# Performance work log

Hardware: AMD Instinct MI355X
Metric: run time of the kernel (lower is better)

Reference implementation:

```python
import jax, jax.numpy as jnp
import numpy as np

NUM_ITEM = 50000
D = 64
LN_EPS = 1e-5


def _l2norm(x, axis=-1):
    # F.normalize: x / max(||x||, eps)
    n = jnp.sqrt(jnp.sum(x * x, axis=axis, keepdims=True))
    return x / jnp.maximum(n, 1e-12)


def _mlp(x, w1, b1, w2, b2, w3, b3):
    h = jax.nn.relu(x @ w1.T + b1)
    h = jax.nn.relu(h @ w2.T + b2)
    return h @ w3.T + b3


def setup_inputs() -> dict:
    key = jax.random.key(0)
    ks = jax.random.split(key, 20)
    d_c, d_t = 1024, 768
    inp = {
        'seq_modify': jax.random.randint(ks[0], (1024, 50), 0, NUM_ITEM + 1),
        'content_feature': jax.random.normal(ks[1], (NUM_ITEM, d_c), jnp.float32),
        'text_feature': jax.random.normal(ks[2], (NUM_ITEM, d_t), jnp.float32),
        'cf_feature': jax.random.normal(ks[3], (NUM_ITEM, D), jnp.float32),
        'item_embeddings': jax.random.normal(ks[4], (NUM_ITEM, D), jnp.float32) * 0.05,
        'c_w1': jax.random.normal(ks[5], (d_c, d_c), jnp.float32) * (1.0 / np.sqrt(d_c)),
        'c_b1': jnp.zeros((d_c,), jnp.float32),
        'c_w2': jax.random.normal(ks[6], (256, d_c), jnp.float32) * (1.0 / np.sqrt(d_c)),
        'c_b2': jnp.zeros((256,), jnp.float32),
        'c_w3': jax.random.normal(ks[7], (D, 256), jnp.float32) * (1.0 / np.sqrt(256)),
        'c_b3': jnp.zeros((D,), jnp.float32),
        't_w1': jax.random.normal(ks[8], (d_t, d_t), jnp.float32) * (1.0 / np.sqrt(d_t)),
        't_b1': jnp.zeros((d_t,), jnp.float32),
        't_w2': jax.random.normal(ks[9], (256, d_t), jnp.float32) * (1.0 / np.sqrt(d_t)),
        't_b2': jnp.zeros((256,), jnp.float32),
        't_w3': jax.random.normal(ks[10], (D, 256), jnp.float32) * (1.0 / np.sqrt(256)),
        't_b3': jnp.zeros((D,), jnp.float32),
        'cf_w': jax.random.normal(ks[11], (D, D), jnp.float32) * (1.0 / np.sqrt(D)),
        'cf_b': jnp.zeros((D,), jnp.float32),
        'wq': jax.random.normal(ks[12], (D, D), jnp.float32) * (1.0 / np.sqrt(D)),
        'wk': jax.random.normal(ks[13], (D, D), jnp.float32) * (1.0 / np.sqrt(D)),
        'wv': jax.random.normal(ks[14], (D, D), jnp.float32) * (1.0 / np.sqrt(D)),
    }
    return inp


def reference(seq_modify, content_feature, text_feature, cf_feature, item_embeddings,
              c_w1, c_b1, c_w2, c_b2, c_w3, c_b3,
              t_w1, t_b1, t_w2, t_b2, t_w3, t_b3,
              cf_w, cf_b, wq, wk, wv):
    # padding index num_item -> 0 (masked_fill in torch forward)
    seq = jnp.where(seq_modify == NUM_ITEM, 0, seq_modify)  # [bs, n_token]

    # modality encoders over the full catalog (content/text L2-normalized in __init__)
    c_emb = _mlp(_l2norm(content_feature), c_w1, c_b1, c_w2, c_b2, c_w3, c_b3)  # [N, 64]
    t_emb = _mlp(_l2norm(text_feature), t_w1, t_b1, t_w2, t_b2, t_w3, t_b3)    # [N, 64]
    cf_emb = cf_feature @ cf_w.T + cf_b                                         # [N, 64]
    id_emb = item_embeddings                                                    # [N, 64]

    # gather per-token modality embeddings and stack modals: [bs, n, 4, 64]
    feats = jnp.stack([c_emb[seq], t_emb[seq], cf_emb[seq], id_emb[seq]], axis=-2)
    bs, n_tok, n_modal, d = feats.shape

    x = _l2norm(feats).reshape(-1, n_modal, d)  # [bs*n, 4, 64]

    # selfAttention: LayerNorm (no affine) -> q,k,v -> softmax attn -> mean pool
    mu = jnp.mean(x, axis=-1, keepdims=True)
    var = jnp.mean((x - mu) ** 2, axis=-1, keepdims=True)
    xn = (x - mu) / jnp.sqrt(var + LN_EPS)
    q = xn @ wq.T
    k = xn @ wk.T
    v = xn @ wv.T
    attn = jax.nn.softmax(jnp.einsum('bmd,bnd->bmn', q * (d ** -0.5), k), axis=-1)
    fused = jnp.einsum('bmn,bnd->bmd', attn, v).mean(axis=-2)  # [bs*n, 64]
    return fused.reshape(bs, n_tok, d)
```

## Files before the change

### kernel.cpp

```cpp
#include <hip/hip_runtime.h>
#include <hip/hip_bf16.h>
#include <type_traits>

typedef __hip_bfloat16 bf16;
typedef __attribute__((ext_vector_type(8))) short short8;
typedef __attribute__((ext_vector_type(4))) float floatx4;

static constexpr int kNumItem = 50000;

__device__ __forceinline__ float bf2f(const bf16 x) { return __bfloat162float(x); }

union alignas(16) Pack8 {
  bf16 b[8];
  short8 s;
};
union alignas(8) Pack4 {
  bf16 b[4];
  short4 s;
};

__device__ __forceinline__ void async_cp16(const void* g, void* l) {
  __builtin_amdgcn_global_load_lds((const __attribute__((address_space(1))) void*)g,
                                   (__attribute__((address_space(3))) void*)l, 16, 0, 0);
}

__device__ __forceinline__ int xcd_swz(int orig, int nwg) {
  const int nx = 8;
  const int q = nwg / nx, r = nwg % nx;
  const int xcd = orig % nx, loc = orig / nx;
  return (xcd < r ? xcd * (q + 1) : r * (q + 1) + (xcd - r) * q) + loc;
}

__global__ __launch_bounds__(256) void row_invnorm(const float* __restrict__ X,
                                                   float* __restrict__ out,
                                                   int M, int K) {
  const int lane = threadIdx.x & 63;
  const int wave = threadIdx.x >> 6;
  const int row = blockIdx.x * 4 + wave;
  if (row >= M) return;
  const float* xr = X + (size_t)row * K;
  float s = 0.f;
  for (int c = lane * 8; c < K; c += 64 * 8) {
    float4 a = *(const float4*)(xr + c);
    float4 b = *(const float4*)(xr + c + 4);
    s += a.x * a.x + a.y * a.y + a.z * a.z + a.w * a.w;
    s += b.x * b.x + b.y * b.y + b.z * b.z + b.w * b.w;
  }
#pragma unroll
  for (int off = 32; off > 0; off >>= 1) s += __shfl_xor(s, off, 64);
  if (lane == 0) out[row] = 1.0f / fmaxf(sqrtf(s), 1e-12f);
}

__global__ __launch_bounds__(256) void cvt_rows_norm(const float* __restrict__ X,
                                                     bf16* __restrict__ Xb,
                                                     float* __restrict__ out,
                                                     int M, int K) {
  const int lane = threadIdx.x & 63;
  const int wave = threadIdx.x >> 6;
  const int row = blockIdx.x * 4 + wave;
  if (row >= M) return;
  const float* xr = X + (size_t)row * K;
  bf16* dr = Xb + (size_t)row * K;
  float s = 0.f;
  for (int c = lane * 8; c < K; c += 64 * 8) {
    float4 a = *(const float4*)(xr + c);
    float4 b = *(const float4*)(xr + c + 4);
    s += a.x * a.x + a.y * a.y + a.z * a.z + a.w * a.w;
    s += b.x * b.x + b.y * b.y + b.z * b.z + b.w * b.w;
    Pack8 p;
    p.b[0] = __float2bfloat16(a.x); p.b[1] = __float2bfloat16(a.y);
    p.b[2] = __float2bfloat16(a.z); p.b[3] = __float2bfloat16(a.w);
    p.b[4] = __float2bfloat16(b.x); p.b[5] = __float2bfloat16(b.y);
    p.b[6] = __float2bfloat16(b.z); p.b[7] = __float2bfloat16(b.w);
    *(short8*)(void*)(dr + c) = p.s;
  }
#pragma unroll
  for (int off = 32; off > 0; off >>= 1) s += __shfl_xor(s, off, 64);
  if (lane == 0) out[row] = 1.0f / fmaxf(sqrtf(s), 1e-12f);
}

static constexpr int kNWSeg = 10;
struct WPack {
  const float* src[kNWSeg];
  int start4[kNWSeg];
  int total4;
};
__global__ __launch_bounds__(256) void cvt_many(WPack p, bf16* __restrict__ dst) {
  int c = blockIdx.x * 256 + threadIdx.x;
  const int stride = gridDim.x * 256;
  for (; c < p.total4; c += stride) {
    int s = 0;
#pragma unroll
    for (int k = 1; k < kNWSeg; k++)
      if (c >= p.start4[k]) s = k;
    const float4 v = ((const float4*)p.src[s])[c - p.start4[s]];
    Pack4 q;
    q.b[0] = __float2bfloat16(v.x); q.b[1] = __float2bfloat16(v.y);
    q.b[2] = __float2bfloat16(v.z); q.b[3] = __float2bfloat16(v.w);
    *(short4*)(void*)(dst + (size_t)c * 4) = q.s;
  }
}

template <int BM, int BN, typename AT, typename BT, typename CT>
__global__ __launch_bounds__(256) void gemm_bt(const AT* __restrict__ A,
                                               const BT* __restrict__ B,
                                               CT* __restrict__ C,
                                               int M, int N, int K,
                                               const float* __restrict__ rowScale,
                                               const float* __restrict__ bias,
                                               int doRelu) {
  constexpr int BK = 32;
  __shared__ __align__(16) bf16 sA[BM * BK];
  __shared__ __align__(16) bf16 sB[BN * BK];
  const int t = threadIdx.x;
  const int lane = t & 63;
  const int wave = t >> 6;
  constexpr int WN = BN / 64;
  const int wm = wave / WN;
  const int wn = wave % WN;
  const int gx = gridDim.x;
  const int wgid = xcd_swz(blockIdx.y * gx + blockIdx.x, gx * gridDim.y);
  const int m0 = (wgid / gx) * BM;
  const int n0 = (wgid % gx) * BN;
  const int lane16 = lane & 15;
  const int quad = lane >> 4;

  floatx4 acc[4][4];
#pragma unroll
  for (int i = 0; i < 4; i++)
#pragma unroll
    for (int j = 0; j < 4; j++) acc[i][j] = (floatx4)0.0f;

  for (int k0 = 0; k0 < K; k0 += BK) {
#pragma unroll
    for (int it = 0; it < BM / 64; ++it) {
      int c = t + 256 * it;
      int row = c >> 2;
      int col = (c & 3) * 8;
      int gr = m0 + row;
      if (gr > M - 1) gr = M - 1;
      if constexpr (std::is_same_v<AT, bf16>) {
        async_cp16(A + (size_t)gr * K + k0 + col, &sA[c * 8]);
      } else {
        const float* src = A + (size_t)gr * K + k0 + col;
        float4 fa = *(const float4*)src;
        float4 fb = *(const float4*)(src + 4);
        Pack8 p;
        p.b[0] = __float2bfloat16(fa.x); p.b[1] = __float2bfloat16(fa.y);
        p.b[2] = __float2bfloat16(fa.z); p.b[3] = __float2bfloat16(fa.w);
        p.b[4] = __float2bfloat16(fb.x); p.b[5] = __float2bfloat16(fb.y);
        p.b[6] = __float2bfloat16(fb.z); p.b[7] = __float2bfloat16(fb.w);
        *(short8*)(void*)&sA[c * 8] = p.s;
      }
    }
#pragma unroll
    for (int it = 0; it < BN / 64; ++it) {
      int c = t + 256 * it;
      int row = c >> 2;
      int col = (c & 3) * 8;
      int gr = n0 + row;
      if (gr > N - 1) gr = N - 1;
      if constexpr (std::is_same_v<BT, bf16>) {
        async_cp16(B + (size_t)gr * K + k0 + col, &sB[c * 8]);
      } else {
        const float* src = B + (size_t)gr * K + k0 + col;
        float4 fa = *(const float4*)src;
        float4 fb = *(const float4*)(src + 4);
        Pack8 p;
        p.b[0] = __float2bfloat16(fa.x); p.b[1] = __float2bfloat16(fa.y);
        p.b[2] = __float2bfloat16(fa.z); p.b[3] = __float2bfloat16(fa.w);
        p.b[4] = __float2bfloat16(fb.x); p.b[5] = __float2bfloat16(fb.y);
        p.b[6] = __float2bfloat16(fb.z); p.b[7] = __float2bfloat16(fb.w);
        *(short8*)(void*)&sB[c * 8] = p.s;
      }
    }
    __syncthreads();

    short8 afr[4], bfr[4];
#pragma unroll
    for (int i = 0; i < 4; i++)
      afr[i] = *(const short8*)(const void*)&sA[(wm * 64 + i * 16 + lane16) * BK + quad * 8];
#pragma unroll
    for (int j = 0; j < 4; j++)
      bfr[j] = *(const short8*)(const void*)&sB[(wn * 64 + j * 16 + lane16) * BK + quad * 8];
#pragma unroll
    for (int i = 0; i < 4; i++)
#pragma unroll
      for (int j = 0; j < 4; j++)
        acc[i][j] = __builtin_amdgcn_mfma_f32_16x16x32_bf16(afr[i], bfr[j], acc[i][j], 0, 0, 0);
    __syncthreads();
  }

#pragma unroll
  for (int i = 0; i < 4; i++) {
#pragma unroll
    for (int j = 0; j < 4; j++) {
      const int col = n0 + wn * 64 + j * 16 + lane16;
      const float bv = bias ? bias[col] : 0.f;
#pragma unroll
      for (int r = 0; r < 4; r++) {
        const int row = m0 + wm * 64 + i * 16 + quad * 4 + r;
        if (row < M) {
          float v = acc[i][j][r];
          if (rowScale) v *= rowScale[row];
          v += bv;
          if (doRelu) v = v > 0.f ? v : 0.f;
          if constexpr (std::is_same_v<CT, bf16>)
            C[(size_t)row * N + col] = __float2bfloat16(v);
          else
            C[(size_t)row * N + col] = v;
        }
      }
    }
  }
}

template <typename CT>
__global__ __launch_bounds__(512) void gemm_bt2(const bf16* __restrict__ A,
                                                const bf16* __restrict__ B,
                                                CT* __restrict__ C,
                                                int M, int N, int K,
                                                const float* __restrict__ rowScale,
                                                const float* __restrict__ bias,
                                                int doRelu) {
  constexpr int BM = 128, BN = 256, BK = 32;
  __shared__ __align__(16) bf16 sA[BM * BK];
  __shared__ __align__(16) bf16 sB[BN * BK];
  const int t = threadIdx.x;
  const int lane = t & 63;
  const int wave = t >> 6;
  const int wm = wave >> 2;
  const int wn = wave & 3;
  const int gx = gridDim.x;
  const int wgid = xcd_swz(blockIdx.y * gx + blockIdx.x, gx * gridDim.y);
  const int m0 = (wgid / gx) * BM;
  const int n0 = (wgid % gx) * BN;
  const int lane16 = lane & 15;
  const int quad = lane >> 4;

  floatx4 acc[4][4];
#pragma unroll
  for (int i = 0; i < 4; i++)
#pragma unroll
    for (int j = 0; j < 4; j++) acc[i][j] = (floatx4)0.0f;

  for (int k0 = 0; k0 < K; k0 += BK) {
    {
      const int c = t;
      const int row = c >> 2;
      const int col = (c & 3) * 8;
      int gr = m0 + row;
      if (gr > M - 1) gr = M - 1;
      async_cp16(A + (size_t)gr * K + k0 + col, &sA[c * 8]);
    }
#pragma unroll
    for (int it = 0; it < 2; ++it) {
      const int c = t + 512 * it;
      const int row = c >> 2;
      const int col = (c & 3) * 8;
      int gr = n0 + row;
      if (gr > N - 1) gr = N - 1;
      async_cp16(B + (size_t)gr * K + k0 + col, &sB[c * 8]);
    }
    __syncthreads();

    short8 afr[4], bfr[4];
#pragma unroll
    for (int i = 0; i < 4; i++)
      afr[i] = *(const short8*)(const void*)&sA[(wm * 64 + i * 16 + lane16) * BK + quad * 8];
#pragma unroll
    for (int j = 0; j < 4; j++)
      bfr[j] = *(const short8*)(const void*)&sB[(wn * 64 + j * 16 + lane16) * BK + quad * 8];
#pragma unroll
    for (int i = 0; i < 4; i++)
#pragma unroll
      for (int j = 0; j < 4; j++)
        acc[i][j] = __builtin_amdgcn_mfma_f32_16x16x32_bf16(afr[i], bfr[j], acc[i][j], 0, 0, 0);
    __syncthreads();
  }

#pragma unroll
  for (int i = 0; i < 4; i++) {
#pragma unroll
    for (int j = 0; j < 4; j++) {
      const int col = n0 + wn * 64 + j * 16 + lane16;
      const float bv = bias ? bias[col] : 0.f;
#pragma unroll
      for (int r = 0; r < 4; r++) {
        const int row = m0 + wm * 64 + i * 16 + quad * 4 + r;
        if (row < M) {
          float v = acc[i][j][r];
          if (rowScale) v *= rowScale[row];
          v += bv;
          if (doRelu) v = v > 0.f ? v : 0.f;
          if constexpr (std::is_same_v<CT, bf16>)
            C[(size_t)row * N + col] = __float2bfloat16(v);
          else
            C[(size_t)row * N + col] = v;
        }
      }
    }
  }
}

__global__ __launch_bounds__(256) void norm_ln(const bf16* __restrict__ c_emb,
                                               const bf16* __restrict__ t_emb,
                                               const bf16* __restrict__ cf_emb,
                                               const float* __restrict__ id_emb,
                                               bf16* __restrict__ Xn, int nItem) {
  const int gid = blockIdx.x * 256 + threadIdx.x;
  const int row = gid >> 4;
  const int d4 = gid & 15;
  if (row >= nItem * 4) return;
  const int item = row >> 2;
  const int m = row & 3;

  float x[4];
  if (m == 3) {
    const float4 f = *(const float4*)(id_emb + (size_t)item * 64 + d4 * 4);
    x[0] = f.x; x[1] = f.y; x[2] = f.z; x[3] = f.w;
  } else {
    const bf16* src = (m == 0) ? c_emb : (m == 1 ? t_emb : cf_emb);
    Pack4 p;
    p.s = *(const short4*)(const void*)(src + (size_t)item * 64 + d4 * 4);
    x[0] = bf2f(p.b[0]); x[1] = bf2f(p.b[1]); x[2] = bf2f(p.b[2]); x[3] = bf2f(p.b[3]);
  }

  float sm = x[0] + x[1] + x[2] + x[3];
  float ss = x[0] * x[0] + x[1] * x[1] + x[2] * x[2] + x[3] * x[3];
#pragma unroll
  for (int off = 1; off < 16; off <<= 1) {
    sm += __shfl_xor(sm, off, 64);
    ss += __shfl_xor(ss, off, 64);
  }
  const float inv = 1.0f / fmaxf(sqrtf(ss), 1e-12f);
  const float mu = sm * inv * (1.0f / 64.0f);
  const float ex2 = ss * inv * inv * (1.0f / 64.0f);
  const float var = ex2 - mu * mu;
  const float rs = rsqrtf(var + 1e-5f);

  Pack4 o;
#pragma unroll
  for (int c = 0; c < 4; c++) o.b[c] = __float2bfloat16((x[c] * inv - mu) * rs);
  *(short4*)(void*)(Xn + (size_t)row * 64 + d4 * 4) = o.s;
}

__global__ __launch_bounds__(256) void attn4(const float* __restrict__ Q,
                                             const float* __restrict__ K,
                                             const float* __restrict__ V,
                                             float* __restrict__ out, int nGroup) {
  const int t = threadIdx.x;
  const int wave = t >> 6;
  const int lane = t & 63;
  const int sub = lane >> 4;
  const int d4 = lane & 15;
  const int group = blockIdx.x * 4 + wave;
  if (group >= nGroup) return;
  const int item = group * 4 + sub;
  const size_t rb = (size_t)item * 4;

  float4 q4[4], k4[4], v4[4];
#pragma unroll
  for (int m = 0; m < 4; m++) {
    q4[m] = *(const float4*)(Q + (rb + m) * 64 + d4 * 4);
    k4[m] = *(const float4*)(K + (rb + m) * 64 + d4 * 4);
    v4[m] = *(const float4*)(V + (rb + m) * 64 + d4 * 4);
  }

  float p[16];
#pragma unroll
  for (int m = 0; m < 4; m++)
#pragma unroll
    for (int n = 0; n < 4; n++)
      p[m * 4 + n] = q4[m].x * k4[n].x + q4[m].y * k4[n].y +
                     q4[m].z * k4[n].z + q4[m].w * k4[n].w;
#pragma unroll
  for (int off = 1; off < 16; off <<= 1)
#pragma unroll
    for (int i = 0; i < 16; i++) p[i] += __shfl_xor(p[i], off, 64);

  float abar[4] = {0, 0, 0, 0};
#pragma unroll
  for (int m = 0; m < 4; m++) {
    const float s0 = p[m * 4 + 0] * 0.125f, s1 = p[m * 4 + 1] * 0.125f;
    const float s2 = p[m * 4 + 2] * 0.125f, s3 = p[m * 4 + 3] * 0.125f;
    const float mx = fmaxf(fmaxf(s0, s1), fmaxf(s2, s3));
    const float e0 = expf(s0 - mx), e1 = expf(s1 - mx);
    const float e2 = expf(s2 - mx), e3 = expf(s3 - mx);
    const float inv = 1.0f / (e0 + e1 + e2 + e3);
    abar[0] += e0 * inv;
    abar[1] += e1 * inv;
    abar[2] += e2 * inv;
    abar[3] += e3 * inv;
  }

  float4 o;
  o.x = 0.25f * (abar[0] * v4[0].x + abar[1] * v4[1].x + abar[2] * v4[2].x + abar[3] * v4[3].x);
  o.y = 0.25f * (abar[0] * v4[0].y + abar[1] * v4[1].y + abar[2] * v4[2].y + abar[3] * v4[3].y);
  o.z = 0.25f * (abar[0] * v4[0].z + abar[1] * v4[1].z + abar[2] * v4[2].z + abar[3] * v4[3].z);
  o.w = 0.25f * (abar[0] * v4[0].w + abar[1] * v4[1].w + abar[2] * v4[2].w + abar[3] * v4[3].w);
  *(float4*)(out + (size_t)item * 64 + d4 * 4) = o;
}

__global__ __launch_bounds__(256, 4) void fuse_attn2(const int* __restrict__ seq,
                                                     const bf16* __restrict__ c_emb,
                                                     const bf16* __restrict__ t_emb,
                                                     const bf16* __restrict__ cf_emb,
                                                     const float* __restrict__ id_emb,
                                                     const float* __restrict__ wq,
                                                     const float* __restrict__ wk,
                                                     const float* __restrict__ wv,
                                                     float* __restrict__ out, int n_tok) {
  __shared__ __align__(16) float4 swc[3072];
  __shared__ float sxn[4][4][64];
  const int t = threadIdx.x;
  const int lane = t & 63;
  const int wave = t >> 6;

  for (int c = t; c < 3072; c += 256) {
    const int mat = c >> 10, rem = c & 1023, d4 = rem >> 6, j = rem & 63;
    const float* W = (mat == 0) ? wq : (mat == 1 ? wk : wv);
    swc[c] = *(const float4*)(W + j * 64 + d4 * 4);
  }
  __syncthreads();

  const int gw = blockIdx.x * 4 + wave;
  const int gstride = gridDim.x * 4;
  for (int token = gw; token < n_tok; token += gstride) {
    int idx = seq ? seq[token] : token;
    if (idx >= kNumItem || idx < 0) idx = 0;

    float x[4];
    x[0] = bf2f(c_emb[(size_t)idx * 64 + lane]);
    x[1] = bf2f(t_emb[(size_t)idx * 64 + lane]);
    x[2] = bf2f(cf_emb[(size_t)idx * 64 + lane]);
    x[3] = id_emb[(size_t)idx * 64 + lane];

#pragma unroll
    for (int m = 0; m < 4; m++) {
      float sm = x[m], ss = x[m] * x[m];
#pragma unroll
      for (int off = 32; off > 0; off >>= 1) {
        sm += __shfl_xor(sm, off, 64);
        ss += __shfl_xor(ss, off, 64);
      }
      const float inv = 1.0f / fmaxf(sqrtf(ss), 1e-12f);
      const float xh = x[m] * inv;
      const float mu = sm * inv * (1.0f / 64.0f);
      const float ex2 = ss * inv * inv * (1.0f / 64.0f);
      const float var = ex2 - mu * mu;
      const float xn = (xh - mu) * rsqrtf(var + 1e-5f);
      x[m] = xn;
      sxn[wave][m][lane] = xn;
    }

    float q[4] = {0, 0, 0, 0}, kk[4] = {0, 0, 0, 0}, v[4] = {0, 0, 0, 0};
#pragma unroll
    for (int d4 = 0; d4 < 16; d4++) {
      const float4 a = swc[d4 * 64 + lane];
      const float4 b = swc[1024 + d4 * 64 + lane];
      const float4 g = swc[2048 + d4 * 64 + lane];
#pragma unroll
      for (int m = 0; m < 4; m++) {
        const float4 xn4 = *(const float4*)&sxn[wave][m][d4 * 4];
        q[m] += xn4.x * a.x + xn4.y * a.y + xn4.z * a.z + xn4.w * a.w;
        kk[m] += xn4.x * b.x + xn4.y * b.y + xn4.z * b.z + xn4.w * b.w;
        v[m] += xn4.x * g.x + xn4.y * g.y + xn4.z * g.z + xn4.w * g.w;
      }
    }

    float p[16];
#pragma unroll
    for (int m = 0; m < 4; m++)
#pragma unroll
      for (int n = 0; n < 4; n++) p[m * 4 + n] = q[m] * kk[n];
#pragma unroll
    for (int off = 1; off < 64; off <<= 1)
#pragma unroll
      for (int i = 0; i < 16; i++) p[i] += __shfl_xor(p[i], off, 64);

    float abar[4] = {0, 0, 0, 0};
#pragma unroll
    for (int m = 0; m < 4; m++) {
      float s0 = p[m * 4 + 0] * 0.125f, s1 = p[m * 4 + 1] * 0.125f;
      float s2 = p[m * 4 + 2] * 0.125f, s3 = p[m * 4 + 3] * 0.125f;
      float mx = fmaxf(fmaxf(s0, s1), fmaxf(s2, s3));
      float e0 = expf(s0 - mx), e1 = expf(s1 - mx), e2 = expf(s2 - mx), e3 = expf(s3 - mx);
      float inv = 1.0f / (e0 + e1 + e2 + e3);
      abar[0] += e0 * inv;
      abar[1] += e1 * inv;
      abar[2] += e2 * inv;
      abar[3] += e3 * inv;
    }
    const float o =
        0.25f * (abar[0] * v[0] + abar[1] * v[1] + abar[2] * v[2] + abar[3] * v[3]);
    out[(size_t)token * 64 + lane] = o;
  }
}

__global__ __launch_bounds__(256) void gather_out(const int* __restrict__ seq,
                                                  const float* __restrict__ fused,
                                                  float* __restrict__ out, int n_tok) {
  const int gid = blockIdx.x * 256 + threadIdx.x;
  if (gid >= n_tok * 16) return;
  const int token = gid >> 4;
  const int c4 = gid & 15;
  int idx = seq[token];
  if (idx >= kNumItem || idx < 0) idx = 0;
  ((float4*)out)[(size_t)token * 16 + c4] = ((const float4*)fused)[(size_t)idx * 16 + c4];
}

extern "C" void kernel_launch(void* const* d_in, const int* in_sizes, int n_in,
                              void* d_out, int out_size, void* d_ws, size_t ws_size,
                              hipStream_t stream) {
  const int* seq = (const int*)d_in[0];
  const float* content = (const float*)d_in[1];
  const float* text = (const float*)d_in[2];
  const float* cf_feat = (const float*)d_in[3];
  const float* item_emb = (const float*)d_in[4];
  const float* c_w1 = (const float*)d_in[5];
  const float* c_b1 = (const float*)d_in[6];
  const float* c_w2 = (const float*)d_in[7];
  const float* c_b2 = (const float*)d_in[8];
  const float* c_w3 = (const float*)d_in[9];
  const float* c_b3 = (const float*)d_in[10];
  const float* t_w1 = (const float*)d_in[11];
  const float* t_b1 = (const float*)d_in[12];
  const float* t_w2 = (const float*)d_in[13];
  const float* t_b2 = (const float*)d_in[14];
  const float* t_w3 = (const float*)d_in[15];
  const float* t_b3 = (const float*)d_in[16];
  const float* cf_w = (const float*)d_in[17];
  const float* cf_b = (const float*)d_in[18];
  const float* wq = (const float*)d_in[19];
  const float* wk = (const float*)d_in[20];
  const float* wv = (const float*)d_in[21];
  float* out = (float*)d_out;

  const int M = kNumItem;
  const int n_tok = in_sizes[0];

  char* w = (char*)d_ws;
  size_t off = 0;
  auto alloc = [&](size_t bytes) -> void* {
    void* p = w + off;
    off += (bytes + 255) & ~(size_t)255;
    return p;
  };
  float* invn_c = (float*)alloc((size_t)M * 4);
  float* invn_t = (float*)alloc((size_t)M * 4);
  bf16* c_emb = (bf16*)alloc((size_t)M * 64 * 2);
  bf16* t_emb = (bf16*)alloc((size_t)M * 64 * 2);
  bf16* cf_emb = (bf16*)alloc((size_t)M * 64 * 2);
  bf16* H1 = (bf16*)alloc((size_t)M * 1024 * 2);
  bf16* H2 = (bf16*)alloc((size_t)M * 256 * 2);

  const int nw[kNWSeg] = {1024 * 1024, 256 * 1024, 64 * 256, 768 * 768, 256 * 768,
                          64 * 256,    64 * 64,    64 * 64,  64 * 64,   64 * 64};
  int wofs[kNWSeg + 1];
  wofs[0] = 0;
  for (int i = 0; i < kNWSeg; i++) wofs[i + 1] = wofs[i] + nw[i];
  bf16* Wb = (bf16*)alloc((size_t)wofs[kNWSeg] * 2);
  const bool useWb = (off <= ws_size);
  bf16* Ab = (bf16*)alloc((size_t)M * 1024 * 2);
  const bool useAb = useWb && (off <= ws_size);
  float* fusedTab = (float*)alloc((size_t)M * 64 * 4);
  const bool useFused = (off <= ws_size);

  const int R = M * 4;
  bf16* Xn = (bf16*)Ab;
  float* Vbuf = (float*)((char*)Ab + (size_t)R * 64 * 2);
  float* Qbuf = (float*)H1;
  float* Kbuf = (float*)((char*)H1 + (size_t)R * 64 * 4);

  if (useWb) {
    WPack p;
    const float* srcs[kNWSeg] = {c_w1, c_w2, c_w3, t_w1, t_w2, t_w3, cf_w, wq, wk, wv};
    for (int i = 0; i < kNWSeg; i++) {
      p.src[i] = srcs[i];
      p.start4[i] = wofs[i] / 4;
    }
    p.total4 = wofs[kNWSeg] / 4;
    cvt_many<<<dim3(2048), dim3(256), 0, stream>>>(p, Wb);
  }

  if (useAb) {
    cvt_rows_norm<<<dim3((M + 3) / 4), dim3(256), 0, stream>>>(content, Ab, invn_c, M, 1024);
    gemm_bt2<bf16><<<dim3(1024 / 256, (M + 127) / 128), dim3(512), 0, stream>>>(
        Ab, Wb + wofs[0], H1, M, 1024, 1024, invn_c, c_b1, 1);
    gemm_bt2<bf16><<<dim3(1, (M + 127) / 128), dim3(512), 0, stream>>>(
        H1, Wb + wofs[1], H2, M, 256, 1024, nullptr, c_b2, 1);
    gemm_bt<256, 64, bf16, bf16, bf16>
        <<<dim3(1, (M + 255) / 256), dim3(256), 0, stream>>>(
            H2, Wb + wofs[2], c_emb, M, 64, 256, nullptr, c_b3, 0);

    cvt_rows_norm<<<dim3((M + 3) / 4), dim3(256), 0, stream>>>(text, Ab, invn_t, M, 768);
    gemm_bt2<bf16><<<dim3(768 / 256, (M + 127) / 128), dim3(512), 0, stream>>>(
        Ab, Wb + wofs[3], H1, M, 768, 768, invn_t, t_b1, 1);
    gemm_bt2<bf16><<<dim3(1, (M + 127) / 128), dim3(512), 0, stream>>>(
        H1, Wb + wofs[4], H2, M, 256, 768, nullptr, t_b2, 1);
    gemm_bt<256, 64, bf16, bf16, bf16>
        <<<dim3(1, (M + 255) / 256), dim3(256), 0, stream>>>(
            H2, Wb + wofs[5], t_emb, M, 64, 256, nullptr, t_b3, 0);

    gemm_bt<256, 64, float, bf16, bf16>
        <<<dim3(1, (M + 255) / 256), dim3(256), 0, stream>>>(
            cf_feat, Wb + wofs[6], cf_emb, M, 64, 64, nullptr, cf_b, 0);

    norm_ln<<<dim3((R * 16 + 255) / 256), dim3(256), 0, stream>>>(
        c_emb, t_emb, cf_emb, item_emb, Xn, M);
    gemm_bt<256, 64, bf16, bf16, float>
        <<<dim3(1, (R + 255) / 256), dim3(256), 0, stream>>>(
            Xn, Wb + wofs[7], Qbuf, R, 64, 64, nullptr, nullptr, 0);
    gemm_bt<256, 64, bf16, bf16, float>
        <<<dim3(1, (R + 255) / 256), dim3(256), 0, stream>>>(
            Xn, Wb + wofs[8], Kbuf, R, 64, 64, nullptr, nullptr, 0);
    gemm_bt<256, 64, bf16, bf16, float>
        <<<dim3(1, (R + 255) / 256), dim3(256), 0, stream>>>(
            Xn, Wb + wofs[9], Vbuf, R, 64, 64, nullptr, nullptr, 0);
    const int nGroup = (M + 3) / 4;
    attn4<<<dim3((nGroup + 3) / 4), dim3(256), 0, stream>>>(
        Qbuf, Kbuf, Vbuf, fusedTab, nGroup);
    gather_out<<<dim3((n_tok * 16 + 255) / 256), dim3(256), 0, stream>>>(
        seq, fusedTab, out, n_tok);
  } else if (useWb) {
    row_invnorm<<<dim3((M + 3) / 4), dim3(256), 0, stream>>>(content, invn_c, M, 1024);
    row_invnorm<<<dim3((M + 3) / 4), dim3(256), 0, stream>>>(text, invn_t, M, 768);
    gemm_bt<128, 128, float, bf16, bf16>
        <<<dim3(1024 / 128, (M + 127) / 128), dim3(256), 0, stream>>>(
            content, Wb + wofs[0], H1, M, 1024, 1024, invn_c, c_b1, 1);
    gemm_bt<128, 128, bf16, bf16, bf16>
        <<<dim3(256 / 128, (M + 127) / 128), dim3(256), 0, stream>>>(
            H1, Wb + wofs[1], H2, M, 256, 1024, nullptr, c_b2, 1);
    gemm_bt<256, 64, bf16, bf16, bf16>
        <<<dim3(1, (M + 255) / 256), dim3(256), 0, stream>>>(
            H2, Wb + wofs[2], c_emb, M, 64, 256, nullptr, c_b3, 0);
    gemm_bt<128, 128, float, bf16, bf16>
        <<<dim3(768 / 128, (M + 127) / 128), dim3(256), 0, stream>>>(
            text, Wb + wofs[3], H1, M, 768, 768, invn_t, t_b1, 1);
    gemm_bt<128, 128, bf16, bf16, bf16>
        <<<dim3(256 / 128, (M + 127) / 128), dim3(256), 0, stream>>>(
            H1, Wb + wofs[4], H2, M, 256, 768, nullptr, t_b2, 1);
    gemm_bt<256, 64, bf16, bf16, bf16>
        <<<dim3(1, (M + 255) / 256), dim3(256), 0, stream>>>(
            H2, Wb + wofs[5], t_emb, M, 64, 256, nullptr, t_b3, 0);
    gemm_bt<256, 64, float, bf16, bf16>
        <<<dim3(1, (M + 255) / 256), dim3(256), 0, stream>>>(
            cf_feat, Wb + wofs[6], cf_emb, M, 64, 64, nullptr, cf_b, 0);
    if (useFused) {
      fuse_attn2<<<dim3(768), dim3(256), 0, stream>>>(
          nullptr, c_emb, t_emb, cf_emb, item_emb, wq, wk, wv, fusedTab, M);
      gather_out<<<dim3((n_tok * 16 + 255) / 256), dim3(256), 0, stream>>>(
          seq, fusedTab, out, n_tok);
    } else {
      fuse_attn2<<<dim3(768), dim3(256), 0, stream>>>(
          seq, c_emb, t_emb, cf_emb, item_emb, wq, wk, wv, out, n_tok);
    }
  } else {
    row_invnorm<<<dim3((M + 3) / 4), dim3(256), 0, stream>>>(content, invn_c, M, 1024);
    row_invnorm<<<dim3((M + 3) / 4), dim3(256), 0, stream>>>(text, invn_t, M, 768);
    gemm_bt<128, 128, float, float, bf16>
        <<<dim3(1024 / 128, (M + 127) / 128), dim3(256), 0, stream>>>(
            content, c_w1, H1, M, 1024, 1024, invn_c, c_b1, 1);
    gemm_bt<128, 128, bf16, float, bf16>
        <<<dim3(256 / 128, (M + 127) / 128), dim3(256), 0, stream>>>(
            H1, c_w2, H2, M, 256, 1024, nullptr, c_b2, 1);
    gemm_bt<256, 64, bf16, float, bf16>
        <<<dim3(1, (M + 255) / 256), dim3(256), 0, stream>>>(
            H2, c_w3, c_emb, M, 64, 256, nullptr, c_b3, 0);
    gemm_bt<128, 128, float, float, bf16>
        <<<dim3(768 / 128, (M + 127) / 128), dim3(256), 0, stream>>>(
            text, t_w1, H1, M, 768, 768, invn_t, t_b1, 1);
    gemm_bt<128, 128, bf16, float, bf16>
        <<<dim3(256 / 128, (M + 127) / 128), dim3(256), 0, stream>>>(
            H1, t_w2, H2, M, 256, 768, nullptr, t_b2, 1);
    gemm_bt<256, 64, bf16, float, bf16>
        <<<dim3(1, (M + 255) / 256), dim3(256), 0, stream>>>(
            H2, t_w3, t_emb, M, 64, 256, nullptr, t_b3, 0);
    gemm_bt<256, 64, float, float, bf16>
        <<<dim3(1, (M + 255) / 256), dim3(256), 0, stream>>>(
            cf_feat, cf_w, cf_emb, M, 64, 64, nullptr, cf_b, 0);
    fuse_attn2<<<dim3(768), dim3(256), 0, stream>>>(
        seq, c_emb, t_emb, cf_emb, item_emb, wq, wk, wv, out, n_tok);
  }
}
```

Measured before the change: 1.034 ms.

## Double-buffer GEMM LDS tiles and merge Q/K projections into one bf16 GEMM

Both GEMM kernels now use two LDS buffers per operand, so the next K-tile is prefetched while MFMAs run on the current one, and one barrier per iteration is dropped. Separately, the Q and K projections become a single GEMM with N=128 over the contiguous wq/wk weights, writing bf16 instead of fp32, and attn4 reads the interleaved QK buffer. This cuts one launch and halves the Q/K intermediate traffic. The cost is doubled LDS usage, which may lower occupancy, and Q/K now carry bf16 precision.

```diff
diff --git a/kernel.cpp b/kernel.cpp
--- a/kernel.cpp
+++ b/kernel.cpp
@@ -110,8 +110,8 @@
                                                const float* __restrict__ bias,
                                                int doRelu) {
   constexpr int BK = 32;
-  __shared__ __align__(16) bf16 sA[BM * BK];
-  __shared__ __align__(16) bf16 sB[BN * BK];
+  __shared__ __align__(16) bf16 sA[2][BM * BK];
+  __shared__ __align__(16) bf16 sB[2][BN * BK];
   const int t = threadIdx.x;
   const int lane = t & 63;
   const int wave = t >> 6;
@@ -125,13 +125,7 @@
   const int lane16 = lane & 15;
   const int quad = lane >> 4;
 
-  floatx4 acc[4][4];
-#pragma unroll
-  for (int i = 0; i < 4; i++)
-#pragma unroll
-    for (int j = 0; j < 4; j++) acc[i][j] = (floatx4)0.0f;
-
-  for (int k0 = 0; k0 < K; k0 += BK) {
+  auto stageA = [&](int k0, bf16* dst) {
 #pragma unroll
     for (int it = 0; it < BM / 64; ++it) {
       int c = t + 256 * it;
@@ -140,7 +134,7 @@
       int gr = m0 + row;
       if (gr > M - 1) gr = M - 1;
       if constexpr (std::is_same_v<AT, bf16>) {
-        async_cp16(A + (size_t)gr * K + k0 + col, &sA[c * 8]);
+        async_cp16(A + (size_t)gr * K + k0 + col, dst + c * 8);
       } else {
         const float* src = A + (size_t)gr * K + k0 + col;
         float4 fa = *(const float4*)src;
@@ -150,9 +144,11 @@
         p.b[2] = __float2bfloat16(fa.z); p.b[3] = __float2bfloat16(fa.w);
         p.b[4] = __float2bfloat16(fb.x); p.b[5] = __float2bfloat16(fb.y);
         p.b[6] = __float2bfloat16(fb.z); p.b[7] = __float2bfloat16(fb.w);
-        *(short8*)(void*)&sA[c * 8] = p.s;
+        *(short8*)(void*)(dst + c * 8) = p.s;
       }
     }
+  };
+  auto stageB = [&](int k0, bf16* dst) {
 #pragma unroll
     for (int it = 0; it < BN / 64; ++it) {
       int c = t + 256 * it;
@@ -161,7 +157,7 @@
       int gr = n0 + row;
       if (gr > N - 1) gr = N - 1;
       if constexpr (std::is_same_v<BT, bf16>) {
-        async_cp16(B + (size_t)gr * K + k0 + col, &sB[c * 8]);
+        async_cp16(B + (size_t)gr * K + k0 + col, dst + c * 8);
       } else {
         const float* src = B + (size_t)gr * K + k0 + col;
         float4 fa = *(const float4*)src;
@@ -171,24 +167,41 @@
         p.b[2] = __float2bfloat16(fa.z); p.b[3] = __float2bfloat16(fa.w);
         p.b[4] = __float2bfloat16(fb.x); p.b[5] = __float2bfloat16(fb.y);
         p.b[6] = __float2bfloat16(fb.z); p.b[7] = __float2bfloat16(fb.w);
-        *(short8*)(void*)&sB[c * 8] = p.s;
+        *(short8*)(void*)(dst + c * 8) = p.s;
       }
     }
-    __syncthreads();
-
+  };
+
+  floatx4 acc[4][4];
+#pragma unroll
+  for (int i = 0; i < 4; i++)
+#pragma unroll
+    for (int j = 0; j < 4; j++) acc[i][j] = (floatx4)0.0f;
+
+  stageA(0, sA[0]);
+  stageB(0, sB[0]);
+  __syncthreads();
+  int cur = 0;
+  for (int k0 = 0; k0 < K; k0 += BK) {
+    const int nxt = cur ^ 1;
+    if (k0 + BK < K) {
+      stageA(k0 + BK, sA[nxt]);
+      stageB(k0 + BK, sB[nxt]);
+    }
     short8 afr[4], bfr[4];
 #pragma unroll
     for (int i = 0; i < 4; i++)
-      afr[i] = *(const short8*)(const void*)&sA[(wm * 64 + i * 16 + lane16) * BK + quad * 8];
+      afr[i] = *(const short8*)(const void*)&sA[cur][(wm * 64 + i * 16 + lane16) * BK + quad * 8];
 #pragma unroll
     for (int j = 0; j < 4; j++)
-      bfr[j] = *(const short8*)(const void*)&sB[(wn * 64 + j * 16 + lane16) * BK + quad * 8];
+      bfr[j] = *(const short8*)(const void*)&sB[cur][(wn * 64 + j * 16 + lane16) * BK + quad * 8];
 #pragma unroll
     for (int i = 0; i < 4; i++)
 #pragma unroll
       for (int j = 0; j < 4; j++)
         acc[i][j] = __builtin_amdgcn_mfma_f32_16x16x32_bf16(afr[i], bfr[j], acc[i][j], 0, 0, 0);
     __syncthreads();
+    cur = nxt;
   }
 
 #pragma unroll
@@ -224,8 +237,8 @@
                                                 const float* __restrict__ bias,
                                                 int doRelu) {
   constexpr int BM = 128, BN = 256, BK = 32;
-  __shared__ __align__(16) bf16 sA[BM * BK];
-  __shared__ __align__(16) bf16 sB[BN * BK];
+  __shared__ __align__(16) bf16 sA[2][BM * BK];
+  __shared__ __align__(16) bf16 sB[2][BN * BK];
   const int t = threadIdx.x;
   const int lane = t & 63;
   const int wave = t >> 6;
@@ -238,20 +251,14 @@
   const int lane16 = lane & 15;
   const int quad = lane >> 4;
 
-  floatx4 acc[4][4];
-#pragma unroll
-  for (int i = 0; i < 4; i++)
-#pragma unroll
-    for (int j = 0; j < 4; j++) acc[i][j] = (floatx4)0.0f;
-
-  for (int k0 = 0; k0 < K; k0 += BK) {
+  auto stage = [&](int k0, bf16* dA, bf16* dB) {
     {
       const int c = t;
       const int row = c >> 2;
       const int col = (c & 3) * 8;
       int gr = m0 + row;
       if (gr > M - 1) gr = M - 1;
-      async_cp16(A + (size_t)gr * K + k0 + col, &sA[c * 8]);
+      async_cp16(A + (size_t)gr * K + k0 + col, dA + c * 8);
     }
 #pragma unroll
     for (int it = 0; it < 2; ++it) {
@@ -260,23 +267,37 @@
       const int col = (c & 3) * 8;
       int gr = n0 + row;
       if (gr > N - 1) gr = N - 1;
-      async_cp16(B + (size_t)gr * K + k0 + col, &sB[c * 8]);
-    }
-    __syncthreads();
+      async_cp16(B + (size_t)gr * K + k0 + col, dB + c * 8);
+    }
+  };
+
+  floatx4 acc[4][4];
+#pragma unroll
+  for (int i = 0; i < 4; i++)
+#pragma unroll
+    for (int j = 0; j < 4; j++) acc[i][j] = (floatx4)0.0f;
+
+  stage(0, sA[0], sB[0]);
+  __syncthreads();
+  int cur = 0;
+  for (int k0 = 0; k0 < K; k0 += BK) {
+    const int nxt = cur ^ 1;
+    if (k0 + BK < K) stage(k0 + BK, sA[nxt], sB[nxt]);
 
     short8 afr[4], bfr[4];
 #pragma unroll
     for (int i = 0; i < 4; i++)
-      afr[i] = *(const short8*)(const void*)&sA[(wm * 64 + i * 16 + lane16) * BK + quad * 8];
+      afr[i] = *(const short8*)(const void*)&sA[cur][(wm * 64 + i * 16 + lane16) * BK + quad * 8];
 #pragma unroll
     for (int j = 0; j < 4; j++)
-      bfr[j] = *(const short8*)(const void*)&sB[(wn * 64 + j * 16 + lane16) * BK + quad * 8];
+      bfr[j] = *(const short8*)(const void*)&sB[cur][(wn * 64 + j * 16 + lane16) * BK + quad * 8];
 #pragma unroll
     for (int i = 0; i < 4; i++)
 #pragma unroll
       for (int j = 0; j < 4; j++)
         acc[i][j] = __builtin_amdgcn_mfma_f32_16x16x32_bf16(afr[i], bfr[j], acc[i][j], 0, 0, 0);
     __syncthreads();
+    cur = nxt;
   }
 
 #pragma unroll
@@ -345,8 +366,7 @@
   *(short4*)(void*)(Xn + (size_t)row * 64 + d4 * 4) = o.s;
 }
 
-__global__ __launch_bounds__(256) void attn4(const float* __restrict__ Q,
-                                             const float* __restrict__ K,
+__global__ __launch_bounds__(256) void attn4(const bf16* __restrict__ QK,
                                              const float* __restrict__ V,
                                              float* __restrict__ out, int nGroup) {
   const int t = threadIdx.x;
@@ -362,8 +382,11 @@
   float4 q4[4], k4[4], v4[4];
 #pragma unroll
   for (int m = 0; m < 4; m++) {
-    q4[m] = *(const float4*)(Q + (rb + m) * 64 + d4 * 4);
-    k4[m] = *(const float4*)(K + (rb + m) * 64 + d4 * 4);
+    Pack4 pq, pk;
+    pq.s = *(const short4*)(const void*)(QK + (rb + m) * 128 + d4 * 4);
+    pk.s = *(const short4*)(const void*)(QK + (rb + m) * 128 + 64 + d4 * 4);
+    q4[m] = float4{bf2f(pq.b[0]), bf2f(pq.b[1]), bf2f(pq.b[2]), bf2f(pq.b[3])};
+    k4[m] = float4{bf2f(pk.b[0]), bf2f(pk.b[1]), bf2f(pk.b[2]), bf2f(pk.b[3])};
     v4[m] = *(const float4*)(V + (rb + m) * 64 + d4 * 4);
   }
 
@@ -570,8 +593,7 @@
   const int R = M * 4;
   bf16* Xn = (bf16*)Ab;
   float* Vbuf = (float*)((char*)Ab + (size_t)R * 64 * 2);
-  float* Qbuf = (float*)H1;
-  float* Kbuf = (float*)((char*)H1 + (size_t)R * 64 * 4);
+  bf16* QKbuf = (bf16*)H1;
 
   if (useWb) {
     WPack p;
@@ -609,18 +631,15 @@
 
     norm_ln<<<dim3((R * 16 + 255) / 256), dim3(256), 0, stream>>>(
         c_emb, t_emb, cf_emb, item_emb, Xn, M);
-    gemm_bt<256, 64, bf16, bf16, float>
-        <<<dim3(1, (R + 255) / 256), dim3(256), 0, stream>>>(
-            Xn, Wb + wofs[7], Qbuf, R, 64, 64, nullptr, nullptr, 0);
-    gemm_bt<256, 64, bf16, bf16, float>
-        <<<dim3(1, (R + 255) / 256), dim3(256), 0, stream>>>(
-            Xn, Wb + wofs[8], Kbuf, R, 64, 64, nullptr, nullptr, 0);
+    gemm_bt<256, 64, bf16, bf16, bf16>
+        <<<dim3(2, (R + 255) / 256), dim3(256), 0, stream>>>(
+            Xn, Wb + wofs[7], QKbuf, R, 128, 64, nullptr, nullptr, 0);
     gemm_bt<256, 64, bf16, bf16, float>
         <<<dim3(1, (R + 255) / 256), dim3(256), 0, stream>>>(
             Xn, Wb + wofs[9], Vbuf, R, 64, 64, nullptr, nullptr, 0);
     const int nGroup = (M + 3) / 4;
     attn4<<<dim3((nGroup + 3) / 4), dim3(256), 0, stream>>>(
-        Qbuf, Kbuf, Vbuf, fusedTab, nGroup);
+        QKbuf, Vbuf, fusedTab, nGroup);
     gather_out<<<dim3((n_tok * 16 + 255) / 256), dim3(256), 0, stream>>>(
         seq, fusedTab, out, n_tok);
   } else if (useWb) {
```

After: 999.0 us. -3.4%, faster.
